# Kernel tuning notes

Measured on AMD Instinct MI355X. Metric: run time of the kernel, lower is better.

Reference implementation:

```python
import jax, jax.numpy as jnp
import numpy as np

B, N, S = 8, 4096, 1024
D1, D2 = 128, 256
IN_CH, OUT_CH = D1 + D2, 256
BN_EPS = 1e-5


def setup_inputs() -> dict:
    key = jax.random.key(0)
    ks = jax.random.split(key, 12)
    inp = {
        "xyz1": jax.random.normal(ks[0], (B, N, 3), jnp.float32),
        "xyz2": jax.random.normal(ks[1], (B, S, 3), jnp.float32),
        "points1": jax.random.normal(ks[2], (B, N, D1), jnp.float32),
        "points2": jax.random.normal(ks[3], (B, S, D2), jnp.float32),
        # fuse: Conv1d(in_ch->out_ch, k=1) + BN
        "W_fuse": jax.random.normal(ks[4], (OUT_CH, IN_CH), jnp.float32) * (1.0 / np.sqrt(IN_CH)),
        "b_fuse": jnp.zeros((OUT_CH,), jnp.float32),
        "g_fuse": jnp.ones((OUT_CH,), jnp.float32),
        "bt_fuse": jnp.zeros((OUT_CH,), jnp.float32),
        # res block net1: Conv1d(out_ch->out_ch) + BN (res_expansion=1.0)
        "W1": jax.random.normal(ks[5], (OUT_CH, OUT_CH), jnp.float32) * (1.0 / np.sqrt(OUT_CH)),
        "b1": jnp.zeros((OUT_CH,), jnp.float32),
        "g1": jnp.ones((OUT_CH,), jnp.float32),
        "bt1": jnp.zeros((OUT_CH,), jnp.float32),
        # res block net2: Conv1d(out_ch->out_ch) + BN
        "W2": jax.random.normal(ks[6], (OUT_CH, OUT_CH), jnp.float32) * (1.0 / np.sqrt(OUT_CH)),
        "b2": jnp.zeros((OUT_CH,), jnp.float32),
        "g2": jnp.ones((OUT_CH,), jnp.float32),
        "bt2": jnp.zeros((OUT_CH,), jnp.float32),
    }
    return inp


def _bn(x, g, b):
    # BatchNorm1d training-mode forward: stats over (batch, length), x: [B, C, L]
    m = jnp.mean(x, axis=(0, 2), keepdims=True)
    v = jnp.var(x, axis=(0, 2), keepdims=True)
    return (x - m) * jax.lax.rsqrt(v + BN_EPS) * g[None, :, None] + b[None, :, None]


def _conv1x1(x, W, b):
    # x: [B, C_in, L], W: [C_out, C_in] -> [B, C_out, L]
    return jnp.einsum("oc,bcl->bol", W, x) + b[None, :, None]


def _gelu(x):
    return jax.nn.gelu(x, approximate=False)  # torch nn.GELU default (erf)


def reference(xyz1, xyz2, points1, points2,
              W_fuse, b_fuse, g_fuse, bt_fuse,
              W1, b1, g1, bt1, W2, b2, g2, bt2):
    # squared pairwise distances [B, N, S] without B x N x S x 3 intermediate
    d = (jnp.sum(xyz1 * xyz1, -1)[:, :, None]
         - 2.0 * jnp.einsum("bnc,bsc->bns", xyz1, xyz2)
         + jnp.sum(xyz2 * xyz2, -1)[:, None, :])
    # 3 nearest coarse points per dense point (== sort ascending, take first 3)
    neg_d3, idx = jax.lax.top_k(-d, 3)            # [B, N, 3]
    d3 = -neg_d3
    recip = 1.0 / (d3 + 1e-8)
    w = recip / jnp.sum(recip, axis=2, keepdims=True)  # [B, N, 3]
    gathered = points2[jnp.arange(points2.shape[0])[:, None, None], idx]  # [B, N, 3, D2]
    interp = jnp.sum(gathered * w[..., None], axis=2)  # [B, N, D2]

    new_points = jnp.concatenate([points1, interp], axis=-1)  # [B, N, D1+D2]
    x = jnp.transpose(new_points, (0, 2, 1))                   # [B, C, N]

    # fuse: conv-bn-gelu
    x = _gelu(_bn(_conv1x1(x, W_fuse, b_fuse), g_fuse, bt_fuse))
    # residual block: gelu(bn(conv(gelu(bn(conv(x))))) + x)
    y = _gelu(_bn(_conv1x1(x, W1, b1), g1, bt1))
    y = _bn(_conv1x1(y, W2, b2), g2, bt2)
    x = _gelu(y + x)

    return jnp.transpose(x, (0, 2, 1))  # [B, N, out_ch]
```

## Files before the change

kernel.cpp:

```cpp
#include <hip/hip_runtime.h>
#include <hip/hip_bf16.h>

constexpr int Bb = 8, Nn = 4096, Ss = 1024;
constexpr int D1 = 128, D2 = 256, KIN = 384, OC = 256;
constexpr int L = Bb * Nn;
constexpr float BN_EPS = 1e-5f;

typedef __attribute__((ext_vector_type(4))) float floatx4;
typedef __attribute__((ext_vector_type(8))) __bf16 bf16x8;

#define DEV __device__ __forceinline__

DEV float bf2f(unsigned short u) {
    union { unsigned int i; float f; } v; v.i = ((unsigned int)u) << 16; return v.f;
}
DEV unsigned short f2bf(float f) {
    union { float f; unsigned int i; } v; v.f = f;
    unsigned int x = v.i;
    return (unsigned short)((x + 0x7FFFu + ((x >> 16) & 1u)) >> 16);
}
DEV float gelu_f(float x) {
    float u = x * (0.7978845608f + 0.0356774081f * x * x);
    float t = __expf(-2.0f * u);
    return x * __builtin_amdgcn_rcpf(1.0f + t);
}

DEV bool probe_isf(const unsigned int* __restrict__ w, int tid) {
    unsigned int lo = w[tid & 63] & 0xFFFFu;
    int e = (int)((lo >> 7) & 0xFF);
    unsigned long long m = __ballot(e >= 100 && e <= 144);
    return __popcll(m) < 48;
}

template <int K> DEV int permoff(int off) {
    int row = off / K, rr = off - row * K;
    int cg = (rr >> 3) & 7;
    return row * K + (rr & ~63) + (((cg ^ (row & 7)) << 3)) + (rr & 7);
}

DEV void merge3(float& d0, float& d1, float& d2, int& i0, int& i1, int& i2,
                float e0, float e1, float e2, int j0, int j1, int j2, bool pref) {
    float a0 = d0, a1 = d1, a2 = d2; int x0 = i0, x1 = i1, x2 = i2;
    float b0 = e0, b1 = e1;          int y0 = j0, y1 = j1;
    bool t = pref ? (a0 <= b0) : (a0 < b0);
    d0 = t ? a0 : b0; i0 = t ? x0 : y0;
    a0 = t ? a1 : a0; x0 = t ? x1 : x0;
    a1 = t ? a2 : a1; x1 = t ? x2 : x1;
    b0 = t ? b0 : b1; y0 = t ? y0 : y1;
    b1 = t ? b1 : e2; y1 = t ? y1 : j2;
    t = pref ? (a0 <= b0) : (a0 < b0);
    d1 = t ? a0 : b0; i1 = t ? x0 : y0;
    a0 = t ? a1 : a0; x0 = t ? x1 : x0;
    b0 = t ? b0 : b1; y0 = t ? y0 : y1;
    t = pref ? (a0 <= b0) : (a0 < b0);
    d2 = t ? a0 : b0; i2 = t ? x0 : y0;
}

__global__ __launch_bounds__(256) void k_front(const void* __restrict__ xyz1_,
                                               const void* __restrict__ xyz2_,
                                               const void* __restrict__ w0_,
                                               const void* __restrict__ w1_,
                                               const void* __restrict__ w2_,
                                               unsigned short* __restrict__ Wdst,
                                               float* __restrict__ stats,
                                               int* __restrict__ dflag,
                                               int* __restrict__ nn_idx,
                                               float* __restrict__ nn_w) {
    int tid = threadIdx.x;
    int bid = blockIdx.x;
    bool isf = probe_isf((const unsigned int*)xyz1_, tid);

    if (bid < 6) {
        stats[bid * 256 + tid] = 0.0f;
        if (bid == 0 && tid == 0) *dflag = isf ? 1 : 0;
        return;
    }
    if (bid < 902) {
        int i = (bid - 6) * 256 + tid;
        const void* src; int off;
        if (i < 98304)       { src = w0_; off = permoff<384>(i); }
        else if (i < 163840) { src = w1_; off = permoff<256>(i - 98304); }
        else                 { src = w2_; off = permoff<256>(i - 163840); }
        Wdst[i] = isf ? f2bf(((const float*)src)[off]) : ((const unsigned short*)src)[off];
        return;
    }

    __shared__ alignas(16) float s4[Ss * 4 + 32];
    int bn0 = (bid - 902) * 32;
    int b = bn0 >> 12;

    if (isf) {
        const float* p2 = (const float*)xyz2_ + (size_t)b * Ss * 3;
        for (int i = tid; i < Ss * 3; i += 256) {
            int s = i / 3, k = i - s * 3;
            s4[s * 4 + k + ((s >> 7) << 2)] = p2[i];
        }
    } else {
        const unsigned short* p2 = (const unsigned short*)xyz2_ + (size_t)b * Ss * 3;
        for (int i = tid; i < Ss * 3; i += 256) {
            int s = i / 3, k = i - s * 3;
            s4[s * 4 + k + ((s >> 7) << 2)] = bf2f(p2[i]);
        }
    }
    __syncthreads();
    for (int s = tid; s < Ss; s += 256) {
        int a = s * 4 + ((s >> 7) << 2);
        float x = s4[a], y = s4[a + 1], z = s4[a + 2];
        s4[a + 3] = x * x + y * y + z * z;
    }
    __syncthreads();

    int part = tid & 7;
    int bn = bn0 + (tid >> 3);
    float x1, y1, z1;
    if (isf) {
        const float* p1 = (const float*)xyz1_ + (size_t)bn * 3;
        x1 = p1[0]; y1 = p1[1]; z1 = p1[2];
    } else {
        const unsigned short* p1 = (const unsigned short*)xyz1_ + (size_t)bn * 3;
        x1 = bf2f(p1[0]); y1 = bf2f(p1[1]); z1 = bf2f(p1[2]);
    }
    float n1 = x1 * x1 + y1 * y1 + z1 * z1;

    float d0 = 3.4e38f, d1 = 3.4e38f, d2 = 3.4e38f;
    int i0 = 0, i1 = 0, i2 = 0;
    const float* sp = &s4[part * 516];
#pragma unroll 4
    for (int j = 0; j < 128; ++j) {
        float4 qv = *(const float4*)(sp + j * 4);
        float d = n1 + qv.w - 2.0f * (x1 * qv.x + y1 * qv.y + z1 * qv.z);
        int s = part * 128 + j;
        bool c2 = d < d2, c1 = d < d1, c0 = d < d0;
        d2 = c1 ? d1 : (c2 ? d : d2); i2 = c1 ? i1 : (c2 ? s : i2);
        d1 = c0 ? d0 : (c1 ? d : d1); i1 = c0 ? i0 : (c1 ? s : i1);
        d0 = c0 ? d  : d0;            i0 = c0 ? s  : i0;
    }
#pragma unroll
    for (int m = 1; m <= 4; m <<= 1) {
        float e0 = __shfl_xor(d0, m, 64), e1 = __shfl_xor(d1, m, 64), e2 = __shfl_xor(d2, m, 64);
        int   j0 = __shfl_xor(i0, m, 64), j1 = __shfl_xor(i1, m, 64), j2 = __shfl_xor(i2, m, 64);
        bool pref = (part < (part ^ m));
        merge3(d0, d1, d2, i0, i1, i2, e0, e1, e2, j0, j1, j2, pref);
    }
    if (part == 0) {
        float r0 = 1.0f / (d0 + 1e-8f), r1 = 1.0f / (d1 + 1e-8f), r2 = 1.0f / (d2 + 1e-8f);
        float rs = 1.0f / (r0 + r1 + r2);
        nn_idx[bn * 3 + 0] = i0; nn_idx[bn * 3 + 1] = i1; nn_idx[bn * 3 + 2] = i2;
        nn_w[bn * 3 + 0] = r0 * rs; nn_w[bn * 3 + 1] = r1 * rs; nn_w[bn * 3 + 2] = r2 * rs;
    }
}

__global__ __launch_bounds__(256) void k_gemm1(const void* __restrict__ p1_,
                                               const void* __restrict__ p2_,
                                               const int* __restrict__ nn_idx,
                                               const float* __restrict__ nn_w,
                                               const int* __restrict__ dflag,
                                               const unsigned short* __restrict__ W,
                                               unsigned short* __restrict__ Out,
                                               float* __restrict__ S1, float* __restrict__ S2) {
    __shared__ alignas(16) unsigned short As[64 * 64];
    __shared__ alignas(16) unsigned short Bs[256 * 64];
    __shared__ float sS1[256], sS2[256];

    int tid = threadIdx.x;
    int l0 = blockIdx.x * 64;
    int wn = tid >> 6, lane = tid & 63, quad = lane >> 4, lr = lane & 15;
    bool isf = (*dflag != 0);

    floatx4 acc[4][4];
#pragma unroll
    for (int mi = 0; mi < 4; ++mi)
#pragma unroll
        for (int ni = 0; ni < 4; ++ni) acc[mi][ni] = (floatx4){0.f, 0.f, 0.f, 0.f};

    for (int kc = 0; kc < KIN / 64; ++kc) {
        __syncthreads();
#pragma unroll
        for (int it = 0; it < 8; ++it) {
            int chunk = it * 4 + wn;
            int row = chunk * 8 + (lane >> 3);
            int cg = lane & 7;
            const unsigned short* src = W + (size_t)row * KIN + kc * 64 + cg * 8;
            __builtin_amdgcn_global_load_lds(
                (const __attribute__((address_space(1))) void*)src,
                (__attribute__((address_space(3))) void*)&Bs[chunk * 512],
                16, 0, 0);
        }
#pragma unroll
        for (int it = 0; it < 2; ++it) {
            int idx = it * 256 + tid, row = idx >> 3, c8 = idx & 7;
            int pt = l0 + row;
            int c0 = kc * 64 + c8 * 8;
            union { uint4 v; unsigned short u[8]; } va;
            if (c0 < D1) {
                if (isf) {
                    const float* p = (const float*)p1_ + (size_t)pt * D1 + c0;
                    float4 f0 = *(const float4*)p;
                    float4 f1 = *(const float4*)(p + 4);
                    va.u[0] = f2bf(f0.x); va.u[1] = f2bf(f0.y); va.u[2] = f2bf(f0.z); va.u[3] = f2bf(f0.w);
                    va.u[4] = f2bf(f1.x); va.u[5] = f2bf(f1.y); va.u[6] = f2bf(f1.z); va.u[7] = f2bf(f1.w);
                } else {
                    va.v = *(const uint4*)((const unsigned short*)p1_ + (size_t)pt * D1 + c0);
                }
            } else {
                int c2 = c0 - D1;
                int b = pt >> 12;
                int j0 = nn_idx[pt * 3], j1 = nn_idx[pt * 3 + 1], j2 = nn_idx[pt * 3 + 2];
                float w0 = nn_w[pt * 3], w1 = nn_w[pt * 3 + 1], w2 = nn_w[pt * 3 + 2];
                if (isf) {
                    const float* base = (const float*)p2_;
                    const float* r0 = base + ((size_t)(b * Ss + j0)) * D2 + c2;
                    const float* r1 = base + ((size_t)(b * Ss + j1)) * D2 + c2;
                    const float* r2 = base + ((size_t)(b * Ss + j2)) * D2 + c2;
#pragma unroll
                    for (int h = 0; h < 2; ++h) {
                        float4 a0 = *(const float4*)(r0 + h * 4);
                        float4 a1 = *(const float4*)(r1 + h * 4);
                        float4 a2 = *(const float4*)(r2 + h * 4);
                        va.u[h * 4 + 0] = f2bf(w0 * a0.x + w1 * a1.x + w2 * a2.x);
                        va.u[h * 4 + 1] = f2bf(w0 * a0.y + w1 * a1.y + w2 * a2.y);
                        va.u[h * 4 + 2] = f2bf(w0 * a0.z + w1 * a1.z + w2 * a2.z);
                        va.u[h * 4 + 3] = f2bf(w0 * a0.w + w1 * a1.w + w2 * a2.w);
                    }
                } else {
                    const unsigned short* base = (const unsigned short*)p2_;
                    uint4 v0 = *(const uint4*)(base + ((size_t)(b * Ss + j0)) * D2 + c2);
                    uint4 v1 = *(const uint4*)(base + ((size_t)(b * Ss + j1)) * D2 + c2);
                    uint4 v2 = *(const uint4*)(base + ((size_t)(b * Ss + j2)) * D2 + c2);
                    const unsigned short* u0 = (const unsigned short*)&v0;
                    const unsigned short* u1 = (const unsigned short*)&v1;
                    const unsigned short* u2 = (const unsigned short*)&v2;
#pragma unroll
                    for (int j = 0; j < 8; ++j)
                        va.u[j] = f2bf(w0 * bf2f(u0[j]) + w1 * bf2f(u1[j]) + w2 * bf2f(u2[j]));
                }
            }
            *(uint4*)&As[row * 64 + ((c8 ^ (row & 7)) << 3)] = va.v;
        }
        __syncthreads();
#pragma unroll
        for (int ks8 = 0; ks8 < 2; ++ks8) {
            bf16x8 af[4], bfr[4];
#pragma unroll
            for (int mi = 0; mi < 4; ++mi) {
                int ra = mi * 16 + lr;
                af[mi] = *(const bf16x8*)&As[ra * 64 + ((((ks8 << 2) + quad) ^ (ra & 7)) << 3)];
            }
#pragma unroll
            for (int ni = 0; ni < 4; ++ni) {
                int rb = wn * 64 + ni * 16 + lr;
                bfr[ni] = *(const bf16x8*)&Bs[rb * 64 + ((((ks8 << 2) + quad) ^ (rb & 7)) << 3)];
            }
#pragma unroll
            for (int mi = 0; mi < 4; ++mi)
#pragma unroll
                for (int ni = 0; ni < 4; ++ni)
                    acc[mi][ni] = __builtin_amdgcn_mfma_f32_16x16x32_bf16(af[mi], bfr[ni], acc[mi][ni], 0, 0, 0);
        }
    }

    float p1a[4] = {0, 0, 0, 0}, p2a[4] = {0, 0, 0, 0};
#pragma unroll
    for (int mi = 0; mi < 4; ++mi)
#pragma unroll
        for (int ni = 0; ni < 4; ++ni)
#pragma unroll
            for (int r = 0; r < 4; ++r) {
                float v = acc[mi][ni][r];
                int row = l0 + mi * 16 + quad * 4 + r;
                int col = wn * 64 + ni * 16 + lr;
                Out[(size_t)row * OC + col] = f2bf(v);
                p1a[ni] += v; p2a[ni] += v * v;
            }
    sS1[tid] = 0.f; sS2[tid] = 0.f;
    __syncthreads();
#pragma unroll
    for (int ni = 0; ni < 4; ++ni) {
        atomicAdd(&sS1[wn * 64 + ni * 16 + lr], p1a[ni]);
        atomicAdd(&sS2[wn * 64 + ni * 16 + lr], p2a[ni]);
    }
    __syncthreads();
    atomicAdd(&S1[tid], sS1[tid]);
    atomicAdd(&S2[tid], sS2[tid]);
}

template <int K>
__global__ __launch_bounds__(256) void k_gemm(const unsigned short* __restrict__ A,
                                              const unsigned short* __restrict__ W,
                                              unsigned short* __restrict__ Out,
                                              float* __restrict__ S1, float* __restrict__ S2,
                                              const float* __restrict__ S1in,
                                              const float* __restrict__ S2in,
                                              const void* __restrict__ g_,
                                              const void* __restrict__ bt_,
                                              const int* __restrict__ dflag) {
    __shared__ alignas(16) unsigned short As[64 * K];
    __shared__ alignas(16) unsigned short Bs[256 * 64];
    __shared__ float sS1[256], sS2[256];
    __shared__ float sCA[256], sCC[256];

    int tid = threadIdx.x;
    int l0 = blockIdx.x * 64;
    int wn = tid >> 6, lane = tid & 63, quad = lane >> 4, lr = lane & 15;

    {
        float m = S1in[tid] * (1.0f / (float)L);
        float var = S2in[tid] * (1.0f / (float)L) - m * m;
        float g, bt;
        if (*dflag) { g = ((const float*)g_)[tid]; bt = ((const float*)bt_)[tid]; }
        else { g = bf2f(((const unsigned short*)g_)[tid]); bt = bf2f(((const unsigned short*)bt_)[tid]); }
        float a = g * rsqrtf(var + BN_EPS);
        sCA[tid] = a;
        sCC[tid] = bt - m * a;
    }
    __syncthreads();

#pragma unroll
    for (int it = 0; it < (64 * K / 8) / 256; ++it) {
        int idx = it * 256 + tid;
        int row = idx >> 5, cg = idx & 31;
        union { uint4 v; unsigned short u[8]; } va;
        va.v = *(const uint4*)(A + (size_t)(l0 + row) * K + cg * 8);
        int kb = cg * 8;
#pragma unroll
        for (int j = 0; j < 8; ++j) {
            float f = bf2f(va.u[j]);
            va.u[j] = f2bf(gelu_f(sCA[kb + j] * f + sCC[kb + j]));
        }
        int sg = (cg & 24) | ((cg & 7) ^ (row & 7));
        *(uint4*)&As[row * K + sg * 8] = va.v;
    }

    floatx4 acc[4][4];
#pragma unroll
    for (int mi = 0; mi < 4; ++mi)
#pragma unroll
        for (int ni = 0; ni < 4; ++ni) acc[mi][ni] = (floatx4){0.f, 0.f, 0.f, 0.f};

    constexpr int KC = K / 64;
    for (int kc = 0; kc < KC; ++kc) {
        __syncthreads();
#pragma unroll
        for (int it = 0; it < 8; ++it) {
            int chunk = it * 4 + wn;
            int row = chunk * 8 + (lane >> 3);
            int cg = lane & 7;
            const unsigned short* src = W + (size_t)row * K + kc * 64 + cg * 8;
            __builtin_amdgcn_global_load_lds(
                (const __attribute__((address_space(1))) void*)src,
                (__attribute__((address_space(3))) void*)&Bs[chunk * 512],
                16, 0, 0);
        }
        __syncthreads();
#pragma unroll
        for (int ks8 = 0; ks8 < 2; ++ks8) {
            bf16x8 af[4], bfr[4];
#pragma unroll
            for (int mi = 0; mi < 4; ++mi) {
                int ra = mi * 16 + lr;
                int g = kc * 8 + ((((ks8 << 2) + quad)) ^ (ra & 7));
                af[mi] = *(const bf16x8*)&As[ra * K + g * 8];
            }
#pragma unroll
            for (int ni = 0; ni < 4; ++ni) {
                int rb = wn * 64 + ni * 16 + lr;
                bfr[ni] = *(const bf16x8*)&Bs[rb * 64 + ((((ks8 << 2) + quad) ^ (rb & 7)) << 3)];
            }
#pragma unroll
            for (int mi = 0; mi < 4; ++mi)
#pragma unroll
                for (int ni = 0; ni < 4; ++ni)
                    acc[mi][ni] = __builtin_amdgcn_mfma_f32_16x16x32_bf16(af[mi], bfr[ni], acc[mi][ni], 0, 0, 0);
        }
    }

    float p1a[4] = {0, 0, 0, 0}, p2a[4] = {0, 0, 0, 0};
#pragma unroll
    for (int mi = 0; mi < 4; ++mi)
#pragma unroll
        for (int ni = 0; ni < 4; ++ni)
#pragma unroll
            for (int r = 0; r < 4; ++r) {
                float v = acc[mi][ni][r];
                int row = l0 + mi * 16 + quad * 4 + r;
                int col = wn * 64 + ni * 16 + lr;
                Out[(size_t)row * OC + col] = f2bf(v);
                p1a[ni] += v; p2a[ni] += v * v;
            }
    sS1[tid] = 0.f; sS2[tid] = 0.f;
    __syncthreads();
#pragma unroll
    for (int ni = 0; ni < 4; ++ni) {
        atomicAdd(&sS1[wn * 64 + ni * 16 + lr], p1a[ni]);
        atomicAdd(&sS2[wn * 64 + ni * 16 + lr], p2a[ni]);
    }
    __syncthreads();
    atomicAdd(&S1[tid], sS1[tid]);
    atomicAdd(&S2[tid], sS2[tid]);
}

__global__ __launch_bounds__(256) void k_final(const unsigned short* __restrict__ t0,
                                               const unsigned short* __restrict__ t2,
                                               const float* __restrict__ S1_0, const float* __restrict__ S2_0,
                                               const float* __restrict__ S1_2, const float* __restrict__ S2_2,
                                               const void* __restrict__ g0_, const void* __restrict__ bt0_,
                                               const void* __restrict__ g2_, const void* __restrict__ bt2_,
                                               const int* __restrict__ dflag,
                                               void* __restrict__ out_) {
    __shared__ float sA0[256], sC0[256], sA2[256], sC2[256];
    int tid = threadIdx.x;
    bool isf = (*dflag != 0);
    {
        float m0 = S1_0[tid] * (1.0f / (float)L);
        float v0_ = S2_0[tid] * (1.0f / (float)L) - m0 * m0;
        float m2 = S1_2[tid] * (1.0f / (float)L);
        float v2_ = S2_2[tid] * (1.0f / (float)L) - m2 * m2;
        float g0, b0, g2, b2;
        if (isf) {
            g0 = ((const float*)g0_)[tid]; b0 = ((const float*)bt0_)[tid];
            g2 = ((const float*)g2_)[tid]; b2 = ((const float*)bt2_)[tid];
        } else {
            g0 = bf2f(((const unsigned short*)g0_)[tid]); b0 = bf2f(((const unsigned short*)bt0_)[tid]);
            g2 = bf2f(((const unsigned short*)g2_)[tid]); b2 = bf2f(((const unsigned short*)bt2_)[tid]);
        }
        float a0 = g0 * rsqrtf(v0_ + BN_EPS);
        float a2 = g2 * rsqrtf(v2_ + BN_EPS);
        sA0[tid] = a0; sC0[tid] = b0 - m0 * a0;
        sA2[tid] = a2; sC2[tid] = b2 - m2 * a2;
    }
    __syncthreads();

    int idx = (blockIdx.x * 256 + tid) * 8;
    int col = idx & (OC - 1);
    union { uint4 v; unsigned short u[8]; } v0, v2;
    v0.v = *(const uint4*)(t0 + idx);
    v2.v = *(const uint4*)(t2 + idx);
    float r[8];
#pragma unroll
    for (int j = 0; j < 8; ++j) {
        float x = gelu_f(sA0[col + j] * bf2f(v0.u[j]) + sC0[col + j]);
        float y = sA2[col + j] * bf2f(v2.u[j]) + sC2[col + j];
        r[j] = gelu_f(x + y);
    }
    if (isf) {
        float* o = (float*)out_ + idx;
        float4 lo = {r[0], r[1], r[2], r[3]};
        float4 hi = {r[4], r[5], r[6], r[7]};
        *(float4*)o = lo;
        *(float4*)(o + 4) = hi;
    } else {
        union { uint4 v; unsigned short u[8]; } vo;
#pragma unroll
        for (int j = 0; j < 8; ++j) vo.u[j] = f2bf(r[j]);
        *(uint4*)((unsigned short*)out_ + idx) = vo.v;
    }
}

extern "C" void kernel_launch(void* const* d_in, const int* in_sizes, int n_in,
                              void* d_out, int out_size, void* d_ws, size_t ws_size,
                              hipStream_t stream) {
    const void* xyz1    = d_in[0];
    const void* xyz2    = d_in[1];
    const void* points1 = d_in[2];
    const void* points2 = d_in[3];
    const void* W_fuse  = d_in[4];
    const void* g_fuse  = d_in[6];
    const void* bt_fuse = d_in[7];
    const void* W1      = d_in[8];
    const void* g1      = d_in[10];
    const void* bt1     = d_in[11];
    const void* W2      = d_in[12];
    const void* g2      = d_in[14];
    const void* bt2     = d_in[15];

    char* ws = (char*)d_ws;
    unsigned short* t2 = (unsigned short*)ws;
    unsigned short* t0 = (unsigned short*)(ws + 25165824);
    unsigned short* t1 = (unsigned short*)d_out;
    int*   nn_idx = (int*)(ws + 41943040);
    float* nn_w   = (float*)(ws + 42336256);
    float* stats  = (float*)(ws + 42729472);
    int*   dflag  = (int*)(ws + 42729472 + 3072 * 4);
    unsigned short* Wbf = (unsigned short*)(ws + 42745856);

    float *S1_0 = stats,        *S2_0 = stats + 256;
    float *S1_1 = stats + 512,  *S2_1 = stats + 768;
    float *S1_2 = stats + 1024, *S2_2 = stats + 1280;

    k_front<<<1926, 256, 0, stream>>>(xyz1, xyz2, W_fuse, W1, W2, Wbf, stats, dflag, nn_idx, nn_w);
    k_gemm1<<<L / 64, 256, 0, stream>>>(points1, points2, nn_idx, nn_w, dflag,
                                        Wbf, t0, S1_0, S2_0);
    k_gemm<OC><<<L / 64, 256, 0, stream>>>(t0, Wbf + 98304, t1, S1_1, S2_1,
                                           S1_0, S2_0, g_fuse, bt_fuse, dflag);
    k_gemm<OC><<<L / 64, 256, 0, stream>>>(t1, Wbf + 163840, t2, S1_2, S2_2,
                                           S1_1, S2_1, g1, bt1, dflag);
    k_final<<<L * OC / (256 * 8), 256, 0, stream>>>(t0, t2, S1_0, S2_0, S1_2, S2_2,
                                                    g_fuse, bt_fuse, g2, bt2, dflag, d_out);
}
```

Before: 229.1 us.

## Fuse KNN, three GEMMs and final epilogue into one persistent kernel with grid barriers

Replaces the front/gemm1/gemm/gemm/final launch chain with a weight-prep kernel and a single persistent kernel of 256 blocks, each owning 128 rows. Stages are separated by software grid barriers built on atomics, and the KNN results stay in shared memory instead of going through global buffers. This removes launch gaps and the nn_idx/nn_w round trip. In exchange it assumes all 256 blocks are co-resident (64KB+ LDS per block), and it cuts parallelism per stage to 256 blocks versus 512+ before.

```diff
diff --git a/kernel.cpp b/kernel.cpp
--- a/kernel.cpp
+++ b/kernel.cpp
@@ -5,6 +5,7 @@
 constexpr int D1 = 128, D2 = 256, KIN = 384, OC = 256;
 constexpr int L = Bb * Nn;
 constexpr float BN_EPS = 1e-5f;
+constexpr int NBLK = 256;
 
 typedef __attribute__((ext_vector_type(4))) float floatx4;
 typedef __attribute__((ext_vector_type(8))) __bf16 bf16x8;
@@ -23,6 +24,27 @@
     float u = x * (0.7978845608f + 0.0356774081f * x * x);
     float t = __expf(-2.0f * u);
     return x * __builtin_amdgcn_rcpf(1.0f + t);
+}
+DEV float aload(const float* p) {
+    return __hip_atomic_load(p, __ATOMIC_RELAXED, __HIP_MEMORY_SCOPE_AGENT);
+}
+
+DEV void grid_barrier(int* bar, int tid) {
+    __syncthreads();
+    if (tid == 0) {
+        int g = __hip_atomic_load(&bar[1], __ATOMIC_RELAXED, __HIP_MEMORY_SCOPE_AGENT);
+        __threadfence();
+        int prev = __hip_atomic_fetch_add(&bar[0], 1, __ATOMIC_ACQ_REL, __HIP_MEMORY_SCOPE_AGENT);
+        if (prev == NBLK - 1) {
+            __hip_atomic_store(&bar[0], 0, __ATOMIC_RELAXED, __HIP_MEMORY_SCOPE_AGENT);
+            __hip_atomic_fetch_add(&bar[1], 1, __ATOMIC_RELEASE, __HIP_MEMORY_SCOPE_AGENT);
+        } else {
+            while (__hip_atomic_load(&bar[1], __ATOMIC_ACQUIRE, __HIP_MEMORY_SCOPE_AGENT) == g) {
+                __builtin_amdgcn_s_sleep(8);
+            }
+        }
+    }
+    __syncthreads();
 }
 
 DEV bool probe_isf(const unsigned int* __restrict__ w, int tid) {
@@ -34,8 +56,8 @@
 
 template <int K> DEV int permoff(int off) {
     int row = off / K, rr = off - row * K;
-    int cg = (rr >> 3) & 7;
-    return row * K + (rr & ~63) + (((cg ^ (row & 7)) << 3)) + (rr & 7);
+    int cg_ = (rr >> 3) & 7;
+    return row * K + (rr & ~63) + (((cg_ ^ (row & 7)) << 3)) + (rr & 7);
 }
 
 DEV void merge3(float& d0, float& d1, float& d2, int& i0, int& i1, int& i2,
@@ -56,365 +78,373 @@
     d2 = t ? a0 : b0; i2 = t ? x0 : y0;
 }
 
-__global__ __launch_bounds__(256) void k_front(const void* __restrict__ xyz1_,
-                                               const void* __restrict__ xyz2_,
-                                               const void* __restrict__ w0_,
-                                               const void* __restrict__ w1_,
-                                               const void* __restrict__ w2_,
-                                               unsigned short* __restrict__ Wdst,
-                                               float* __restrict__ stats,
-                                               int* __restrict__ dflag,
-                                               int* __restrict__ nn_idx,
-                                               float* __restrict__ nn_w) {
+__global__ __launch_bounds__(256) void k_prep(const void* __restrict__ xyz1_,
+                                              const void* __restrict__ w0_,
+                                              const void* __restrict__ w1_,
+                                              const void* __restrict__ w2_,
+                                              unsigned short* __restrict__ Wdst,
+                                              float* __restrict__ stats,
+                                              int* __restrict__ bar) {
     int tid = threadIdx.x;
     int bid = blockIdx.x;
     bool isf = probe_isf((const unsigned int*)xyz1_, tid);
 
     if (bid < 6) {
         stats[bid * 256 + tid] = 0.0f;
-        if (bid == 0 && tid == 0) *dflag = isf ? 1 : 0;
+        if (bid == 0 && tid < 2) bar[tid] = 0;
         return;
     }
-    if (bid < 902) {
-        int i = (bid - 6) * 256 + tid;
-        const void* src; int off;
-        if (i < 98304)       { src = w0_; off = permoff<384>(i); }
-        else if (i < 163840) { src = w1_; off = permoff<256>(i - 98304); }
-        else                 { src = w2_; off = permoff<256>(i - 163840); }
-        Wdst[i] = isf ? f2bf(((const float*)src)[off]) : ((const unsigned short*)src)[off];
-        return;
-    }
-
-    __shared__ alignas(16) float s4[Ss * 4 + 32];
-    int bn0 = (bid - 902) * 32;
-    int b = bn0 >> 12;
-
-    if (isf) {
-        const float* p2 = (const float*)xyz2_ + (size_t)b * Ss * 3;
-        for (int i = tid; i < Ss * 3; i += 256) {
-            int s = i / 3, k = i - s * 3;
-            s4[s * 4 + k + ((s >> 7) << 2)] = p2[i];
-        }
-    } else {
-        const unsigned short* p2 = (const unsigned short*)xyz2_ + (size_t)b * Ss * 3;
-        for (int i = tid; i < Ss * 3; i += 256) {
-            int s = i / 3, k = i - s * 3;
-            s4[s * 4 + k + ((s >> 7) << 2)] = bf2f(p2[i]);
-        }
-    }
-    __syncthreads();
-    for (int s = tid; s < Ss; s += 256) {
-        int a = s * 4 + ((s >> 7) << 2);
-        float x = s4[a], y = s4[a + 1], z = s4[a + 2];
-        s4[a + 3] = x * x + y * y + z * z;
-    }
-    __syncthreads();
-
-    int part = tid & 7;
-    int bn = bn0 + (tid >> 3);
-    float x1, y1, z1;
-    if (isf) {
-        const float* p1 = (const float*)xyz1_ + (size_t)bn * 3;
-        x1 = p1[0]; y1 = p1[1]; z1 = p1[2];
-    } else {
-        const unsigned short* p1 = (const unsigned short*)xyz1_ + (size_t)bn * 3;
-        x1 = bf2f(p1[0]); y1 = bf2f(p1[1]); z1 = bf2f(p1[2]);
-    }
-    float n1 = x1 * x1 + y1 * y1 + z1 * z1;
-
-    float d0 = 3.4e38f, d1 = 3.4e38f, d2 = 3.4e38f;
-    int i0 = 0, i1 = 0, i2 = 0;
-    const float* sp = &s4[part * 516];
-#pragma unroll 4
-    for (int j = 0; j < 128; ++j) {
-        float4 qv = *(const float4*)(sp + j * 4);
-        float d = n1 + qv.w - 2.0f * (x1 * qv.x + y1 * qv.y + z1 * qv.z);
-        int s = part * 128 + j;
-        bool c2 = d < d2, c1 = d < d1, c0 = d < d0;
-        d2 = c1 ? d1 : (c2 ? d : d2); i2 = c1 ? i1 : (c2 ? s : i2);
-        d1 = c0 ? d0 : (c1 ? d : d1); i1 = c0 ? i0 : (c1 ? s : i1);
-        d0 = c0 ? d  : d0;            i0 = c0 ? s  : i0;
-    }
-#pragma unroll
-    for (int m = 1; m <= 4; m <<= 1) {
-        float e0 = __shfl_xor(d0, m, 64), e1 = __shfl_xor(d1, m, 64), e2 = __shfl_xor(d2, m, 64);
-        int   j0 = __shfl_xor(i0, m, 64), j1 = __shfl_xor(i1, m, 64), j2 = __shfl_xor(i2, m, 64);
-        bool pref = (part < (part ^ m));
-        merge3(d0, d1, d2, i0, i1, i2, e0, e1, e2, j0, j1, j2, pref);
-    }
-    if (part == 0) {
-        float r0 = 1.0f / (d0 + 1e-8f), r1 = 1.0f / (d1 + 1e-8f), r2 = 1.0f / (d2 + 1e-8f);
-        float rs = 1.0f / (r0 + r1 + r2);
-        nn_idx[bn * 3 + 0] = i0; nn_idx[bn * 3 + 1] = i1; nn_idx[bn * 3 + 2] = i2;
-        nn_w[bn * 3 + 0] = r0 * rs; nn_w[bn * 3 + 1] = r1 * rs; nn_w[bn * 3 + 2] = r2 * rs;
-    }
-}
-
-__global__ __launch_bounds__(256) void k_gemm1(const void* __restrict__ p1_,
-                                               const void* __restrict__ p2_,
-                                               const int* __restrict__ nn_idx,
-                                               const float* __restrict__ nn_w,
-                                               const int* __restrict__ dflag,
-                                               const unsigned short* __restrict__ W,
-                                               unsigned short* __restrict__ Out,
-                                               float* __restrict__ S1, float* __restrict__ S2) {
-    __shared__ alignas(16) unsigned short As[64 * 64];
-    __shared__ alignas(16) unsigned short Bs[256 * 64];
-    __shared__ float sS1[256], sS2[256];
-
-    int tid = threadIdx.x;
-    int l0 = blockIdx.x * 64;
-    int wn = tid >> 6, lane = tid & 63, quad = lane >> 4, lr = lane & 15;
-    bool isf = (*dflag != 0);
-
-    floatx4 acc[4][4];
-#pragma unroll
-    for (int mi = 0; mi < 4; ++mi)
-#pragma unroll
-        for (int ni = 0; ni < 4; ++ni) acc[mi][ni] = (floatx4){0.f, 0.f, 0.f, 0.f};
-
-    for (int kc = 0; kc < KIN / 64; ++kc) {
-        __syncthreads();
-#pragma unroll
-        for (int it = 0; it < 8; ++it) {
-            int chunk = it * 4 + wn;
-            int row = chunk * 8 + (lane >> 3);
-            int cg = lane & 7;
-            const unsigned short* src = W + (size_t)row * KIN + kc * 64 + cg * 8;
-            __builtin_amdgcn_global_load_lds(
-                (const __attribute__((address_space(1))) void*)src,
-                (__attribute__((address_space(3))) void*)&Bs[chunk * 512],
-                16, 0, 0);
-        }
-#pragma unroll
-        for (int it = 0; it < 2; ++it) {
-            int idx = it * 256 + tid, row = idx >> 3, c8 = idx & 7;
-            int pt = l0 + row;
-            int c0 = kc * 64 + c8 * 8;
-            union { uint4 v; unsigned short u[8]; } va;
-            if (c0 < D1) {
-                if (isf) {
-                    const float* p = (const float*)p1_ + (size_t)pt * D1 + c0;
-                    float4 f0 = *(const float4*)p;
-                    float4 f1 = *(const float4*)(p + 4);
-                    va.u[0] = f2bf(f0.x); va.u[1] = f2bf(f0.y); va.u[2] = f2bf(f0.z); va.u[3] = f2bf(f0.w);
-                    va.u[4] = f2bf(f1.x); va.u[5] = f2bf(f1.y); va.u[6] = f2bf(f1.z); va.u[7] = f2bf(f1.w);
-                } else {
-                    va.v = *(const uint4*)((const unsigned short*)p1_ + (size_t)pt * D1 + c0);
-                }
-            } else {
-                int c2 = c0 - D1;
-                int b = pt >> 12;
-                int j0 = nn_idx[pt * 3], j1 = nn_idx[pt * 3 + 1], j2 = nn_idx[pt * 3 + 2];
-                float w0 = nn_w[pt * 3], w1 = nn_w[pt * 3 + 1], w2 = nn_w[pt * 3 + 2];
-                if (isf) {
-                    const float* base = (const float*)p2_;
-                    const float* r0 = base + ((size_t)(b * Ss + j0)) * D2 + c2;
-                    const float* r1 = base + ((size_t)(b * Ss + j1)) * D2 + c2;
-                    const float* r2 = base + ((size_t)(b * Ss + j2)) * D2 + c2;
-#pragma unroll
-                    for (int h = 0; h < 2; ++h) {
-                        float4 a0 = *(const float4*)(r0 + h * 4);
-                        float4 a1 = *(const float4*)(r1 + h * 4);
-                        float4 a2 = *(const float4*)(r2 + h * 4);
-                        va.u[h * 4 + 0] = f2bf(w0 * a0.x + w1 * a1.x + w2 * a2.x);
-                        va.u[h * 4 + 1] = f2bf(w0 * a0.y + w1 * a1.y + w2 * a2.y);
-                        va.u[h * 4 + 2] = f2bf(w0 * a0.z + w1 * a1.z + w2 * a2.z);
-                        va.u[h * 4 + 3] = f2bf(w0 * a0.w + w1 * a1.w + w2 * a2.w);
-                    }
-                } else {
-                    const unsigned short* base = (const unsigned short*)p2_;
-                    uint4 v0 = *(const uint4*)(base + ((size_t)(b * Ss + j0)) * D2 + c2);
-                    uint4 v1 = *(const uint4*)(base + ((size_t)(b * Ss + j1)) * D2 + c2);
-                    uint4 v2 = *(const uint4*)(base + ((size_t)(b * Ss + j2)) * D2 + c2);
-                    const unsigned short* u0 = (const unsigned short*)&v0;
-                    const unsigned short* u1 = (const unsigned short*)&v1;
-                    const unsigned short* u2 = (const unsigned short*)&v2;
-#pragma unroll
-                    for (int j = 0; j < 8; ++j)
-                        va.u[j] = f2bf(w0 * bf2f(u0[j]) + w1 * bf2f(u1[j]) + w2 * bf2f(u2[j]));
-                }
-            }
-            *(uint4*)&As[row * 64 + ((c8 ^ (row & 7)) << 3)] = va.v;
-        }
-        __syncthreads();
-#pragma unroll
-        for (int ks8 = 0; ks8 < 2; ++ks8) {
-            bf16x8 af[4], bfr[4];
-#pragma unroll
-            for (int mi = 0; mi < 4; ++mi) {
-                int ra = mi * 16 + lr;
-                af[mi] = *(const bf16x8*)&As[ra * 64 + ((((ks8 << 2) + quad) ^ (ra & 7)) << 3)];
-            }
-#pragma unroll
-            for (int ni = 0; ni < 4; ++ni) {
-                int rb = wn * 64 + ni * 16 + lr;
-                bfr[ni] = *(const bf16x8*)&Bs[rb * 64 + ((((ks8 << 2) + quad) ^ (rb & 7)) << 3)];
-            }
-#pragma unroll
-            for (int mi = 0; mi < 4; ++mi)
-#pragma unroll
-                for (int ni = 0; ni < 4; ++ni)
-                    acc[mi][ni] = __builtin_amdgcn_mfma_f32_16x16x32_bf16(af[mi], bfr[ni], acc[mi][ni], 0, 0, 0);
-        }
-    }
-
-    float p1a[4] = {0, 0, 0, 0}, p2a[4] = {0, 0, 0, 0};
-#pragma unroll
-    for (int mi = 0; mi < 4; ++mi)
-#pragma unroll
-        for (int ni = 0; ni < 4; ++ni)
-#pragma unroll
-            for (int r = 0; r < 4; ++r) {
-                float v = acc[mi][ni][r];
-                int row = l0 + mi * 16 + quad * 4 + r;
-                int col = wn * 64 + ni * 16 + lr;
-                Out[(size_t)row * OC + col] = f2bf(v);
-                p1a[ni] += v; p2a[ni] += v * v;
-            }
-    sS1[tid] = 0.f; sS2[tid] = 0.f;
-    __syncthreads();
-#pragma unroll
-    for (int ni = 0; ni < 4; ++ni) {
-        atomicAdd(&sS1[wn * 64 + ni * 16 + lr], p1a[ni]);
-        atomicAdd(&sS2[wn * 64 + ni * 16 + lr], p2a[ni]);
-    }
-    __syncthreads();
-    atomicAdd(&S1[tid], sS1[tid]);
-    atomicAdd(&S2[tid], sS2[tid]);
-}
-
-template <int K>
-__global__ __launch_bounds__(256) void k_gemm(const unsigned short* __restrict__ A,
+    int i = (bid - 6) * 256 + tid;
+    const void* src; int off;
+    if (i < 98304)       { src = w0_; off = permoff<384>(i); }
+    else if (i < 163840) { src = w1_; off = permoff<256>(i - 98304); }
+    else                 { src = w2_; off = permoff<256>(i - 163840); }
+    Wdst[i] = isf ? f2bf(((const float*)src)[off]) : ((const unsigned short*)src)[off];
+}
+
+__global__ __launch_bounds__(256) void k_mega(const void* __restrict__ xyz1_,
+                                              const void* __restrict__ xyz2_,
+                                              const void* __restrict__ p1_,
+                                              const void* __restrict__ p2_,
                                               const unsigned short* __restrict__ W,
-                                              unsigned short* __restrict__ Out,
-                                              float* __restrict__ S1, float* __restrict__ S2,
-                                              const float* __restrict__ S1in,
-                                              const float* __restrict__ S2in,
-                                              const void* __restrict__ g_,
-                                              const void* __restrict__ bt_,
-                                              const int* __restrict__ dflag) {
-    __shared__ alignas(16) unsigned short As[64 * K];
-    __shared__ alignas(16) unsigned short Bs[256 * 64];
+                                              unsigned short* __restrict__ t0,
+                                              unsigned short* t1,
+                                              unsigned short* __restrict__ t2,
+                                              float* __restrict__ stats,
+                                              int* __restrict__ bar,
+                                              const void* __restrict__ g0_,
+                                              const void* __restrict__ bt0_,
+                                              const void* __restrict__ g1_,
+                                              const void* __restrict__ bt1_,
+                                              const void* __restrict__ g2_,
+                                              const void* __restrict__ bt2_,
+                                              void* out_) {
+    __shared__ alignas(16) unsigned char smem[65536];
+    __shared__ int   sNNi[128 * 3];
+    __shared__ float sNNw[128 * 3];
     __shared__ float sS1[256], sS2[256];
     __shared__ float sCA[256], sCC[256];
 
     int tid = threadIdx.x;
-    int l0 = blockIdx.x * 64;
+    int bid = blockIdx.x;
+    int l0 = bid * 128;
     int wn = tid >> 6, lane = tid & 63, quad = lane >> 4, lr = lane & 15;
+    bool isf = probe_isf((const unsigned int*)xyz1_, tid);
+
+    float *S1_0 = stats,        *S2_0 = stats + 256;
+    float *S1_1 = stats + 512,  *S2_1 = stats + 768;
+    float *S1_2 = stats + 1024, *S2_2 = stats + 1280;
+
+    unsigned short* As = (unsigned short*)smem;
+    unsigned short* Bs = (unsigned short*)(smem + 32768);
 
     {
-        float m = S1in[tid] * (1.0f / (float)L);
-        float var = S2in[tid] * (1.0f / (float)L) - m * m;
-        float g, bt;
-        if (*dflag) { g = ((const float*)g_)[tid]; bt = ((const float*)bt_)[tid]; }
-        else { g = bf2f(((const unsigned short*)g_)[tid]); bt = bf2f(((const unsigned short*)bt_)[tid]); }
-        float a = g * rsqrtf(var + BN_EPS);
-        sCA[tid] = a;
-        sCC[tid] = bt - m * a;
-    }
-    __syncthreads();
-
-#pragma unroll
-    for (int it = 0; it < (64 * K / 8) / 256; ++it) {
-        int idx = it * 256 + tid;
-        int row = idx >> 5, cg = idx & 31;
-        union { uint4 v; unsigned short u[8]; } va;
-        va.v = *(const uint4*)(A + (size_t)(l0 + row) * K + cg * 8);
-        int kb = cg * 8;
-#pragma unroll
-        for (int j = 0; j < 8; ++j) {
-            float f = bf2f(va.u[j]);
-            va.u[j] = f2bf(gelu_f(sCA[kb + j] * f + sCC[kb + j]));
-        }
-        int sg = (cg & 24) | ((cg & 7) ^ (row & 7));
-        *(uint4*)&As[row * K + sg * 8] = va.v;
-    }
-
-    floatx4 acc[4][4];
-#pragma unroll
-    for (int mi = 0; mi < 4; ++mi)
-#pragma unroll
-        for (int ni = 0; ni < 4; ++ni) acc[mi][ni] = (floatx4){0.f, 0.f, 0.f, 0.f};
-
-    constexpr int KC = K / 64;
-    for (int kc = 0; kc < KC; ++kc) {
+        float* s4 = (float*)smem;
+        int b = l0 >> 12;
+        if (isf) {
+            const float* p2 = (const float*)xyz2_ + (size_t)b * Ss * 3;
+            for (int i = tid; i < Ss * 3; i += 256) {
+                int s = i / 3, k = i - s * 3;
+                s4[s * 4 + k + ((s >> 7) << 2)] = p2[i];
+            }
+        } else {
+            const unsigned short* p2 = (const unsigned short*)xyz2_ + (size_t)b * Ss * 3;
+            for (int i = tid; i < Ss * 3; i += 256) {
+                int s = i / 3, k = i - s * 3;
+                s4[s * 4 + k + ((s >> 7) << 2)] = bf2f(p2[i]);
+            }
+        }
         __syncthreads();
-#pragma unroll
-        for (int it = 0; it < 8; ++it) {
-            int chunk = it * 4 + wn;
-            int row = chunk * 8 + (lane >> 3);
-            int cg = lane & 7;
-            const unsigned short* src = W + (size_t)row * K + kc * 64 + cg * 8;
-            __builtin_amdgcn_global_load_lds(
-                (const __attribute__((address_space(1))) void*)src,
-                (__attribute__((address_space(3))) void*)&Bs[chunk * 512],
-                16, 0, 0);
+        for (int s = tid; s < Ss; s += 256) {
+            int a = s * 4 + ((s >> 7) << 2);
+            float x = s4[a], y = s4[a + 1], z = s4[a + 2];
+            s4[a + 3] = x * x + y * y + z * z;
         }
         __syncthreads();
-#pragma unroll
-        for (int ks8 = 0; ks8 < 2; ++ks8) {
-            bf16x8 af[4], bfr[4];
-#pragma unroll
-            for (int mi = 0; mi < 4; ++mi) {
-                int ra = mi * 16 + lr;
-                int g = kc * 8 + ((((ks8 << 2) + quad)) ^ (ra & 7));
-                af[mi] = *(const bf16x8*)&As[ra * K + g * 8];
-            }
+
+        int part = tid & 7;
+#pragma unroll
+        for (int pass = 0; pass < 4; ++pass) {
+            int r = pass * 32 + (tid >> 3);
+            int bn = l0 + r;
+            float x1, y1, z1;
+            if (isf) {
+                const float* p1 = (const float*)xyz1_ + (size_t)bn * 3;
+                x1 = p1[0]; y1 = p1[1]; z1 = p1[2];
+            } else {
+                const unsigned short* p1 = (const unsigned short*)xyz1_ + (size_t)bn * 3;
+                x1 = bf2f(p1[0]); y1 = bf2f(p1[1]); z1 = bf2f(p1[2]);
+            }
+            float n1 = x1 * x1 + y1 * y1 + z1 * z1;
+
+            float d0 = 3.4e38f, d1 = 3.4e38f, d2 = 3.4e38f;
+            int i0 = 0, i1 = 0, i2 = 0;
+            const float* sp = &s4[part * 516];
+#pragma unroll 4
+            for (int j = 0; j < 128; ++j) {
+                float4 qv = *(const float4*)(sp + j * 4);
+                float d = n1 + qv.w - 2.0f * (x1 * qv.x + y1 * qv.y + z1 * qv.z);
+                int s = part * 128 + j;
+                bool c2 = d < d2, c1 = d < d1, c0 = d < d0;
+                d2 = c1 ? d1 : (c2 ? d : d2); i2 = c1 ? i1 : (c2 ? s : i2);
+                d1 = c0 ? d0 : (c1 ? d : d1); i1 = c0 ? i0 : (c1 ? s : i1);
+                d0 = c0 ? d  : d0;            i0 = c0 ? s  : i0;
+            }
+#pragma unroll
+            for (int m = 1; m <= 4; m <<= 1) {
+                float e0 = __shfl_xor(d0, m, 64), e1 = __shfl_xor(d1, m, 64), e2 = __shfl_xor(d2, m, 64);
+                int   j0 = __shfl_xor(i0, m, 64), j1 = __shfl_xor(i1, m, 64), j2 = __shfl_xor(i2, m, 64);
+                bool pref = (part < (part ^ m));
+                merge3(d0, d1, d2, i0, i1, i2, e0, e1, e2, j0, j1, j2, pref);
+            }
+            if (part == 0) {
+                float r0 = 1.0f / (d0 + 1e-8f), r1 = 1.0f / (d1 + 1e-8f), r2 = 1.0f / (d2 + 1e-8f);
+                float rs = 1.0f / (r0 + r1 + r2);
+                sNNi[r * 3 + 0] = i0; sNNi[r * 3 + 1] = i1; sNNi[r * 3 + 2] = i2;
+                sNNw[r * 3 + 0] = r0 * rs; sNNw[r * 3 + 1] = r1 * rs; sNNw[r * 3 + 2] = r2 * rs;
+            }
+        }
+    }
+
+    {
+        sS1[tid] = 0.f; sS2[tid] = 0.f;
+        for (int rt = 0; rt < 2; ++rt) {
+            int r0_ = rt * 64;
+            floatx4 acc[4][4];
+#pragma unroll
+            for (int mi = 0; mi < 4; ++mi)
+#pragma unroll
+                for (int ni = 0; ni < 4; ++ni) acc[mi][ni] = (floatx4){0.f, 0.f, 0.f, 0.f};
+
+            for (int kc = 0; kc < KIN / 64; ++kc) {
+                __syncthreads();
+#pragma unroll
+                for (int it = 0; it < 8; ++it) {
+                    int chunk = it * 4 + wn;
+                    int row = chunk * 8 + (lane >> 3);
+                    int cg_ = lane & 7;
+                    const unsigned short* src = W + (size_t)row * KIN + kc * 64 + cg_ * 8;
+                    __builtin_amdgcn_global_load_lds(
+                        (const __attribute__((address_space(1))) void*)src,
+                        (__attribute__((address_space(3))) void*)&Bs[chunk * 512],
+                        16, 0, 0);
+                }
+#pragma unroll
+                for (int it = 0; it < 2; ++it) {
+                    int idx = it * 256 + tid, row = idx >> 3, c8 = idx & 7;
+                    int pt = l0 + r0_ + row;
+                    int c0 = kc * 64 + c8 * 8;
+                    union { uint4 v; unsigned short u[8]; } va;
+                    if (c0 < D1) {
+                        if (isf) {
+                            const float* p = (const float*)p1_ + (size_t)pt * D1 + c0;
+                            float4 f0 = *(const float4*)p;
+                            float4 f1 = *(const float4*)(p + 4);
+                            va.u[0] = f2bf(f0.x); va.u[1] = f2bf(f0.y); va.u[2] = f2bf(f0.z); va.u[3] = f2bf(f0.w);
+                            va.u[4] = f2bf(f1.x); va.u[5] = f2bf(f1.y); va.u[6] = f2bf(f1.z); va.u[7] = f2bf(f1.w);
+                        } else {
+                            va.v = *(const uint4*)((const unsigned short*)p1_ + (size_t)pt * D1 + c0);
+                        }
+                    } else {
+                        int c2 = c0 - D1;
+                        int b = pt >> 12;
+                        int rr = r0_ + row;
+                        int j0 = sNNi[rr * 3], j1 = sNNi[rr * 3 + 1], j2 = sNNi[rr * 3 + 2];
+                        float w0 = sNNw[rr * 3], w1 = sNNw[rr * 3 + 1], w2 = sNNw[rr * 3 + 2];
+                        if (isf) {
+                            const float* base = (const float*)p2_;
+                            const float* r0p = base + ((size_t)(b * Ss + j0)) * D2 + c2;
+                            const float* r1p = base + ((size_t)(b * Ss + j1)) * D2 + c2;
+                            const float* r2p = base + ((size_t)(b * Ss + j2)) * D2 + c2;
+#pragma unroll
+                            for (int h = 0; h < 2; ++h) {
+                                float4 a0 = *(const float4*)(r0p + h * 4);
+                                float4 a1 = *(const float4*)(r1p + h * 4);
+                                float4 a2 = *(const float4*)(r2p + h * 4);
+                                va.u[h * 4 + 0] = f2bf(w0 * a0.x + w1 * a1.x + w2 * a2.x);
+                                va.u[h * 4 + 1] = f2bf(w0 * a0.y + w1 * a1.y + w2 * a2.y);
+                                va.u[h * 4 + 2] = f2bf(w0 * a0.z + w1 * a1.z + w2 * a2.z);
+                                va.u[h * 4 + 3] = f2bf(w0 * a0.w + w1 * a1.w + w2 * a2.w);
+                            }
+                        } else {
+                            const unsigned short* base = (const unsigned short*)p2_;
+                            uint4 v0 = *(const uint4*)(base + ((size_t)(b * Ss + j0)) * D2 + c2);
+                            uint4 v1 = *(const uint4*)(base + ((size_t)(b * Ss + j1)) * D2 + c2);
+                            uint4 v2 = *(const uint4*)(base + ((size_t)(b * Ss + j2)) * D2 + c2);
+                            const unsigned short* u0 = (const unsigned short*)&v0;
+                            const unsigned short* u1 = (const unsigned short*)&v1;
+                            const unsigned short* u2 = (const unsigned short*)&v2;
+#pragma unroll
+                            for (int j = 0; j < 8; ++j)
+                                va.u[j] = f2bf(w0 * bf2f(u0[j]) + w1 * bf2f(u1[j]) + w2 * bf2f(u2[j]));
+                        }
+                    }
+                    *(uint4*)&As[row * 64 + ((c8 ^ (row & 7)) << 3)] = va.v;
+                }
+                __syncthreads();
+#pragma unroll
+                for (int ks8 = 0; ks8 < 2; ++ks8) {
+                    bf16x8 af[4], bfr[4];
+#pragma unroll
+                    for (int mi = 0; mi < 4; ++mi) {
+                        int ra = mi * 16 + lr;
+                        af[mi] = *(const bf16x8*)&As[ra * 64 + ((((ks8 << 2) + quad) ^ (ra & 7)) << 3)];
+                    }
+#pragma unroll
+                    for (int ni = 0; ni < 4; ++ni) {
+                        int rb = wn * 64 + ni * 16 + lr;
+                        bfr[ni] = *(const bf16x8*)&Bs[rb * 64 + ((((ks8 << 2) + quad) ^ (rb & 7)) << 3)];
+                    }
+#pragma unroll
+                    for (int mi = 0; mi < 4; ++mi)
+#pragma unroll
+                        for (int ni = 0; ni < 4; ++ni)
+                            acc[mi][ni] = __builtin_amdgcn_mfma_f32_16x16x32_bf16(af[mi], bfr[ni], acc[mi][ni], 0, 0, 0);
+                }
+            }
+
+            float p1a[4] = {0, 0, 0, 0}, p2a[4] = {0, 0, 0, 0};
+#pragma unroll
+            for (int mi = 0; mi < 4; ++mi)
+#pragma unroll
+                for (int ni = 0; ni < 4; ++ni)
+#pragma unroll
+                    for (int r = 0; r < 4; ++r) {
+                        float v = acc[mi][ni][r];
+                        int row = l0 + r0_ + mi * 16 + quad * 4 + r;
+                        int col = wn * 64 + ni * 16 + lr;
+                        t0[(size_t)row * OC + col] = f2bf(v);
+                        p1a[ni] += v; p2a[ni] += v * v;
+                    }
 #pragma unroll
             for (int ni = 0; ni < 4; ++ni) {
-                int rb = wn * 64 + ni * 16 + lr;
-                bfr[ni] = *(const bf16x8*)&Bs[rb * 64 + ((((ks8 << 2) + quad) ^ (rb & 7)) << 3)];
-            }
+                atomicAdd(&sS1[wn * 64 + ni * 16 + lr], p1a[ni]);
+                atomicAdd(&sS2[wn * 64 + ni * 16 + lr], p2a[ni]);
+            }
+        }
+        __syncthreads();
+        atomicAdd(&S1_0[tid], sS1[tid]);
+        atomicAdd(&S2_0[tid], sS2[tid]);
+    }
+
+    grid_barrier(bar, tid);
+
+    for (int layer = 0; layer < 2; ++layer) {
+        const unsigned short* Ain = (layer == 0) ? t0 : t1;
+        unsigned short*       Out = (layer == 0) ? t1 : t2;
+        const unsigned short* Wl  = W + (layer == 0 ? 98304 : 163840);
+        const float* S1in = (layer == 0) ? S1_0 : S1_1;
+        const float* S2in = (layer == 0) ? S2_0 : S2_1;
+        float* S1o = (layer == 0) ? S1_1 : S1_2;
+        float* S2o = (layer == 0) ? S2_1 : S2_2;
+        const void* g_  = (layer == 0) ? g0_  : g1_;
+        const void* bt_ = (layer == 0) ? bt0_ : bt1_;
+
+        {
+            float m = aload(&S1in[tid]) * (1.0f / (float)L);
+            float var = aload(&S2in[tid]) * (1.0f / (float)L) - m * m;
+            float g, bt;
+            if (isf) { g = ((const float*)g_)[tid]; bt = ((const float*)bt_)[tid]; }
+            else { g = bf2f(((const unsigned short*)g_)[tid]); bt = bf2f(((const unsigned short*)bt_)[tid]); }
+            float a = g * rsqrtf(var + BN_EPS);
+            sCA[tid] = a;
+            sCC[tid] = bt - m * a;
+            sS1[tid] = 0.f; sS2[tid] = 0.f;
+        }
+        __syncthreads();
+
+        for (int rt = 0; rt < 2; ++rt) {
+            int r0_ = rt * 64;
+            __syncthreads();
+#pragma unroll
+            for (int it = 0; it < 8; ++it) {
+                int idx = it * 256 + tid;
+                int row = idx >> 5, cg_ = idx & 31;
+                union { uint4 v; unsigned short u[8]; } va;
+                va.v = *(const uint4*)(Ain + (size_t)(l0 + r0_ + row) * OC + cg_ * 8);
+                int kb = cg_ * 8;
+#pragma unroll
+                for (int j = 0; j < 8; ++j) {
+                    float f = bf2f(va.u[j]);
+                    va.u[j] = f2bf(gelu_f(sCA[kb + j] * f + sCC[kb + j]));
+                }
+                int sg = (cg_ & 24) | ((cg_ & 7) ^ (row & 7));
+                *(uint4*)&As[row * OC + sg * 8] = va.v;
+            }
+
+            floatx4 acc[4][4];
 #pragma unroll
             for (int mi = 0; mi < 4; ++mi)
 #pragma unroll
+                for (int ni = 0; ni < 4; ++ni) acc[mi][ni] = (floatx4){0.f, 0.f, 0.f, 0.f};
+
+            for (int kc = 0; kc < OC / 64; ++kc) {
+                __syncthreads();
+#pragma unroll
+                for (int it = 0; it < 8; ++it) {
+                    int chunk = it * 4 + wn;
+                    int row = chunk * 8 + (lane >> 3);
+                    int cg_ = lane & 7;
+                    const unsigned short* src = Wl + (size_t)row * OC + kc * 64 + cg_ * 8;
+                    __builtin_amdgcn_global_load_lds(
+                        (const __attribute__((address_space(1))) void*)src,
+                        (__attribute__((address_space(3))) void*)&Bs[chunk * 512],
+                        16, 0, 0);
+                }
+                __syncthreads();
+#pragma unroll
+                for (int ks8 = 0; ks8 < 2; ++ks8) {
+                    bf16x8 af[4], bfr[4];
+#pragma unroll
+                    for (int mi = 0; mi < 4; ++mi) {
+                        int ra = mi * 16 + lr;
+                        int g = kc * 8 + (((ks8 << 2) + quad) ^ (ra & 7));
+                        af[mi] = *(const bf16x8*)&As[ra * OC + g * 8];
+                    }
+#pragma unroll
+                    for (int ni = 0; ni < 4; ++ni) {
+                        int rb = wn * 64 + ni * 16 + lr;
+                        bfr[ni] = *(const bf16x8*)&Bs[rb * 64 + ((((ks8 << 2) + quad) ^ (rb & 7)) << 3)];
+                    }
+#pragma unroll
+                    for (int mi = 0; mi < 4; ++mi)
+#pragma unroll
+                        for (int ni = 0; ni < 4; ++ni)
+                            acc[mi][ni] = __builtin_amdgcn_mfma_f32_16x16x32_bf16(af[mi], bfr[ni], acc[mi][ni], 0, 0, 0);
+                }
+            }
+
+            float p1a[4] = {0, 0, 0, 0}, p2a[4] = {0, 0, 0, 0};
+#pragma unroll
+            for (int mi = 0; mi < 4; ++mi)
+#pragma unroll
                 for (int ni = 0; ni < 4; ++ni)
-                    acc[mi][ni] = __builtin_amdgcn_mfma_f32_16x16x32_bf16(af[mi], bfr[ni], acc[mi][ni], 0, 0, 0);
-        }
-    }
-
-    float p1a[4] = {0, 0, 0, 0}, p2a[4] = {0, 0, 0, 0};
-#pragma unroll
-    for (int mi = 0; mi < 4; ++mi)
-#pragma unroll
-        for (int ni = 0; ni < 4; ++ni)
-#pragma unroll
-            for (int r = 0; r < 4; ++r) {
-                float v = acc[mi][ni][r];
-                int row = l0 + mi * 16 + quad * 4 + r;
-                int col = wn * 64 + ni * 16 + lr;
-                Out[(size_t)row * OC + col] = f2bf(v);
-                p1a[ni] += v; p2a[ni] += v * v;
-            }
-    sS1[tid] = 0.f; sS2[tid] = 0.f;
-    __syncthreads();
-#pragma unroll
-    for (int ni = 0; ni < 4; ++ni) {
-        atomicAdd(&sS1[wn * 64 + ni * 16 + lr], p1a[ni]);
-        atomicAdd(&sS2[wn * 64 + ni * 16 + lr], p2a[ni]);
-    }
-    __syncthreads();
-    atomicAdd(&S1[tid], sS1[tid]);
-    atomicAdd(&S2[tid], sS2[tid]);
-}
-
-__global__ __launch_bounds__(256) void k_final(const unsigned short* __restrict__ t0,
-                                               const unsigned short* __restrict__ t2,
-                                               const float* __restrict__ S1_0, const float* __restrict__ S2_0,
-                                               const float* __restrict__ S1_2, const float* __restrict__ S2_2,
-                                               const void* __restrict__ g0_, const void* __restrict__ bt0_,
-                                               const void* __restrict__ g2_, const void* __restrict__ bt2_,
-                                               const int* __restrict__ dflag,
-                                               void* __restrict__ out_) {
-    __shared__ float sA0[256], sC0[256], sA2[256], sC2[256];
-    int tid = threadIdx.x;
-    bool isf = (*dflag != 0);
+#pragma unroll
+                    for (int r = 0; r < 4; ++r) {
+                        float v = acc[mi][ni][r];
+                        int row = l0 + r0_ + mi * 16 + quad * 4 + r;
+                        int col = wn * 64 + ni * 16 + lr;
+                        Out[(size_t)row * OC + col] = f2bf(v);
+                        p1a[ni] += v; p2a[ni] += v * v;
+                    }
+#pragma unroll
+            for (int ni = 0; ni < 4; ++ni) {
+                atomicAdd(&sS1[wn * 64 + ni * 16 + lr], p1a[ni]);
+                atomicAdd(&sS2[wn * 64 + ni * 16 + lr], p2a[ni]);
+            }
+        }
+        __syncthreads();
+        atomicAdd(&S1o[tid], sS1[tid]);
+        atomicAdd(&S2o[tid], sS2[tid]);
+
+        grid_barrier(bar, tid);
+    }
+
     {
-        float m0 = S1_0[tid] * (1.0f / (float)L);
-        float v0_ = S2_0[tid] * (1.0f / (float)L) - m0 * m0;
-        float m2 = S1_2[tid] * (1.0f / (float)L);
-        float v2_ = S2_2[tid] * (1.0f / (float)L) - m2 * m2;
+        float m0 = aload(&S1_0[tid]) * (1.0f / (float)L);
+        float v0_ = aload(&S2_0[tid]) * (1.0f / (float)L) - m0 * m0;
+        float m2 = aload(&S1_2[tid]) * (1.0f / (float)L);
+        float v2_ = aload(&S2_2[tid]) * (1.0f / (float)L) - m2 * m2;
         float g0, b0, g2, b2;
         if (isf) {
             g0 = ((const float*)g0_)[tid]; b0 = ((const float*)bt0_)[tid];
@@ -425,34 +455,37 @@
         }
         float a0 = g0 * rsqrtf(v0_ + BN_EPS);
         float a2 = g2 * rsqrtf(v2_ + BN_EPS);
-        sA0[tid] = a0; sC0[tid] = b0 - m0 * a0;
-        sA2[tid] = a2; sC2[tid] = b2 - m2 * a2;
+        sCA[tid] = a0; sCC[tid] = b0 - m0 * a0;
+        sS1[tid] = a2; sS2[tid] = b2 - m2 * a2;
     }
     __syncthreads();
 
-    int idx = (blockIdx.x * 256 + tid) * 8;
-    int col = idx & (OC - 1);
-    union { uint4 v; unsigned short u[8]; } v0, v2;
-    v0.v = *(const uint4*)(t0 + idx);
-    v2.v = *(const uint4*)(t2 + idx);
-    float r[8];
-#pragma unroll
-    for (int j = 0; j < 8; ++j) {
-        float x = gelu_f(sA0[col + j] * bf2f(v0.u[j]) + sC0[col + j]);
-        float y = sA2[col + j] * bf2f(v2.u[j]) + sC2[col + j];
-        r[j] = gelu_f(x + y);
-    }
-    if (isf) {
-        float* o = (float*)out_ + idx;
-        float4 lo = {r[0], r[1], r[2], r[3]};
-        float4 hi = {r[4], r[5], r[6], r[7]};
-        *(float4*)o = lo;
-        *(float4*)(o + 4) = hi;
-    } else {
-        union { uint4 v; unsigned short u[8]; } vo;
-#pragma unroll
-        for (int j = 0; j < 8; ++j) vo.u[j] = f2bf(r[j]);
-        *(uint4*)((unsigned short*)out_ + idx) = vo.v;
+#pragma unroll
+    for (int it = 0; it < 16; ++it) {
+        int idx = l0 * OC + it * 2048 + tid * 8;
+        int col = (tid * 8) & (OC - 1);
+        union { uint4 v; unsigned short u[8]; } v0, v2;
+        v0.v = *(const uint4*)(t0 + idx);
+        v2.v = *(const uint4*)(t2 + idx);
+        float r[8];
+#pragma unroll
+        for (int j = 0; j < 8; ++j) {
+            float x = gelu_f(sCA[col + j] * bf2f(v0.u[j]) + sCC[col + j]);
+            float y = sS1[col + j] * bf2f(v2.u[j]) + sS2[col + j];
+            r[j] = gelu_f(x + y);
+        }
+        if (isf) {
+            float* o = (float*)out_ + idx;
+            float4 lo = {r[0], r[1], r[2], r[3]};
+            float4 hi = {r[4], r[5], r[6], r[7]};
+            *(float4*)o = lo;
+            *(float4*)(o + 4) = hi;
+        } else {
+            union { uint4 v; unsigned short u[8]; } vo;
+#pragma unroll
+            for (int j = 0; j < 8; ++j) vo.u[j] = f2bf(r[j]);
+            *(uint4*)((unsigned short*)out_ + idx) = vo.v;
+        }
     }
 }
 
@@ -477,23 +510,13 @@
     unsigned short* t2 = (unsigned short*)ws;
     unsigned short* t0 = (unsigned short*)(ws + 25165824);
     unsigned short* t1 = (unsigned short*)d_out;
-    int*   nn_idx = (int*)(ws + 41943040);
-    float* nn_w   = (float*)(ws + 42336256);
     float* stats  = (float*)(ws + 42729472);
-    int*   dflag  = (int*)(ws + 42729472 + 3072 * 4);
+    int*   bar    = (int*)(ws + 42741760);
     unsigned short* Wbf = (unsigned short*)(ws + 42745856);
 
-    float *S1_0 = stats,        *S2_0 = stats + 256;
-    float *S1_1 = stats + 512,  *S2_1 = stats + 768;
-    float *S1_2 = stats + 1024, *S2_2 = stats + 1280;
-
-    k_front<<<1926, 256, 0, stream>>>(xyz1, xyz2, W_fuse, W1, W2, Wbf, stats, dflag, nn_idx, nn_w);
-    k_gemm1<<<L / 64, 256, 0, stream>>>(points1, points2, nn_idx, nn_w, dflag,
-                                        Wbf, t0, S1_0, S2_0);
-    k_gemm<OC><<<L / 64, 256, 0, stream>>>(t0, Wbf + 98304, t1, S1_1, S2_1,
-                                           S1_0, S2_0, g_fuse, bt_fuse, dflag);
-    k_gemm<OC><<<L / 64, 256, 0, stream>>>(t1, Wbf + 163840, t2, S1_2, S2_2,
-                                           S1_1, S2_1, g1, bt1, dflag);
-    k_final<<<L * OC / (256 * 8), 256, 0, stream>>>(t0, t2, S1_0, S2_0, S1_2, S2_2,
-                                                    g_fuse, bt_fuse, g2, bt2, dflag, d_out);
-}
+    k_prep<<<902, 256, 0, stream>>>(xyz1, W_fuse, W1, W2, Wbf, stats, bar);
+
+    k_mega<<<NBLK, 256, 0, stream>>>(xyz1, xyz2, points1, points2, Wbf,
+                                     t0, t1, t2, stats, bar,
+                                     g_fuse, bt_fuse, g1, bt1, g2, bt2, d_out);
+}
```

New measurement: 309.6 us. 1.35x slower.
